# Performance work log

Hardware: AMD Instinct MI355X
Metric: run time of the kernel (lower is better)

The kernel has to match this reference:

```python
import jax, jax.numpy as jnp
import numpy as np

B, T, C = 4, 2048, 1024
H, DQK, DV = 16, 64, 64
W_SCALE = 0.02  # keep logits in a sane range (mimics GPT-style init)


def setup_inputs() -> dict:
    key = jax.random.key(0)
    k1, k2, k3, k4, k5 = jax.random.split(key, 5)
    x = jax.random.normal(k1, (B, T, C), dtype=jnp.float32)
    Wq = jax.random.normal(k2, (C, H * DQK), dtype=jnp.float32) * W_SCALE
    Wk = jax.random.normal(k3, (C, H * DQK), dtype=jnp.float32) * W_SCALE
    Wv = jax.random.normal(k4, (C, H * DV), dtype=jnp.float32) * W_SCALE
    Wp = jax.random.normal(k5, (DV, C), dtype=jnp.float32) * W_SCALE
    return {"x": x, "Wq": Wq, "Wk": Wk, "Wv": Wv, "Wp": Wp, "iter_num": 0}


def reference(x, Wq, Wk, Wv, Wp, iter_num):
    b, t, c = x.shape
    # projections, split into heads: [B, H, T, D]
    q = (x @ Wq).reshape(b, t, H, DQK).transpose(0, 2, 1, 3)
    k = (x @ Wk).reshape(b, t, H, DQK).transpose(0, 2, 1, 3)
    v = (x @ Wv).reshape(b, t, H, DV).transpose(0, 2, 1, 3)
    scale = 1.0 / jnp.sqrt(jnp.asarray(DQK, dtype=x.dtype))
    att = jnp.einsum('bhqd,bhkd->bhqk', q, k) * scale  # [B,H,T,T]
    causal = jnp.tril(jnp.ones((t, t), dtype=bool))
    att = jnp.where(causal[None, None, :, :], att, -jnp.inf)
    att = jax.nn.softmax(att, axis=-1)
    # att @ v then SUM over heads (not concat): [B, T, DV]
    y = jnp.einsum('bhqk,bhkd->bqd', att, v)
    return y @ Wp  # [B, T, C]
```

## Files before the change

kernel.cpp:

```cpp
#include <hip/hip_runtime.h>
#include <hip/hip_bf16.h>

#define DEVI __device__ __forceinline__

typedef __bf16 bf16x8 __attribute__((ext_vector_type(8)));
typedef float f32x4 __attribute__((ext_vector_type(4)));

DEVI unsigned short f2bf(float x) {
    union { __hip_bfloat16 h; unsigned short u; } v;
    v.h = __float2bfloat16(x);
    return v.u;
}

DEVI float exp2_fast(float x) {
#if __has_builtin(__builtin_amdgcn_exp2f)
    return __builtin_amdgcn_exp2f(x);
#else
    return exp2f(x);
#endif
}

DEVI void gload16(const void* gsrc, void* lds) {
    __builtin_amdgcn_global_load_lds(
        (const __attribute__((address_space(1))) void*)gsrc,
        (__attribute__((address_space(3))) void*)lds,
        16, 0, 0);
}

#define BARRIER_MEM() asm volatile("s_barrier" ::: "memory")
#define WAITVM(n) asm volatile("s_waitcnt vmcnt(" #n ")" ::: "memory")
#define LGKM0() asm volatile("s_waitcnt lgkmcnt(0)" ::: "memory")


__global__ __launch_bounds__(256) void convert_f32_bf16_vec(
    const float* __restrict__ in, unsigned short* __restrict__ out, int n4) {
    int i = blockIdx.x * 256 + threadIdx.x;
    if (i >= n4) return;
    float4 v = reinterpret_cast<const float4*>(in)[i];
    ushort4 o;
    o.x = f2bf(v.x); o.y = f2bf(v.y); o.z = f2bf(v.z); o.w = f2bf(v.w);
    reinterpret_cast<ushort4*>(out)[i] = o;
}

__global__ __launch_bounds__(256) void transpose_wqkv(
    const float* __restrict__ wq, const float* __restrict__ wk,
    const float* __restrict__ wv, unsigned short* __restrict__ dst) {
    __shared__ unsigned short tile[32][33];
    const float* src = (blockIdx.z == 0) ? wq : (blockIdx.z == 1) ? wk : wv;
    unsigned short* d = dst + blockIdx.z * 1024 * 1024;
    int c0 = blockIdx.x * 32, r0 = blockIdx.y * 32;
    int tx = threadIdx.x & 31, ty = threadIdx.x >> 5;
    #pragma unroll
    for (int i = ty; i < 32; i += 8)
        tile[tx][i] = f2bf(src[(r0 + i) * 1024 + c0 + tx]);
    __syncthreads();
    #pragma unroll
    for (int i = ty; i < 32; i += 8)
        d[(c0 + i) * 1024 + r0 + tx] = tile[i][tx];
}

__global__ __launch_bounds__(256) void transpose_f32_to_bf16t(
    const float* __restrict__ src, unsigned short* __restrict__ dst,
    int R, int Cc) {
    __shared__ unsigned short tile[32][33];
    int c0 = blockIdx.x * 32, r0 = blockIdx.y * 32;
    int tx = threadIdx.x & 31, ty = threadIdx.x >> 5;
    #pragma unroll
    for (int i = ty; i < 32; i += 8)
        tile[tx][i] = f2bf(src[(r0 + i) * Cc + c0 + tx]);
    __syncthreads();
    #pragma unroll
    for (int i = ty; i < 32; i += 8)
        dst[(c0 + i) * R + r0 + tx] = tile[i][tx];
}

#define LOAD_A8(mh) do { \
    _Pragma("unroll") \
    for (int q = 0; q < 4; ++q) { \
        a[q][0] = *(const bf16x8*)(Arow + ((mh) * 64 + q * 16) * 128 + p16_0); \
        a[q][1] = *(const bf16x8*)(Arow + ((mh) * 64 + q * 16) * 128 + p16_1); \
    } } while (0)

#define LOAD_B4(nh) do { \
    _Pragma("unroll") \
    for (int q2 = 0; q2 < 2; ++q2) { \
        b##nh[q2][0] = *(const bf16x8*)(Brow + ((nh) * 32 + q2 * 16) * 128 + p16_0); \
        b##nh[q2][1] = *(const bf16x8*)(Brow + ((nh) * 32 + q2 * 16) * 128 + p16_1); \
    } } while (0)

#define QUAD(mh, nh) do { \
    __builtin_amdgcn_s_setprio(1); \
    _Pragma("unroll") \
    for (int q = 0; q < 4; ++q) { \
        _Pragma("unroll") \
        for (int q2 = 0; q2 < 2; ++q2) { \
            acc[(mh) * 4 + q][(nh) * 2 + q2] = __builtin_amdgcn_mfma_f32_16x16x32_bf16( \
                a[q][0], b##nh[q2][0], acc[(mh) * 4 + q][(nh) * 2 + q2], 0, 0, 0); \
            acc[(mh) * 4 + q][(nh) * 2 + q2] = __builtin_amdgcn_mfma_f32_16x16x32_bf16( \
                a[q][1], b##nh[q2][1], acc[(mh) * 4 + q][(nh) * 2 + q2], 0, 0, 0); \
        } } \
    __builtin_amdgcn_s_setprio(0); } while (0)

__global__ __launch_bounds__(512, 2) void gemm256(
    const unsigned short* __restrict__ A, const unsigned short* __restrict__ Bt,
    unsigned short* __restrict__ q_out, unsigned short* __restrict__ k_out,
    unsigned short* __restrict__ v_out) {
    __shared__ unsigned short Ab[2][256 * 64];
    __shared__ unsigned short Bb[2][256 * 64];

    const int wg = (blockIdx.x & 7) * 48 + (blockIdx.x >> 3);
    const int bm = (wg / 12) << 8;
    const int bn = (wg % 12) << 8;

    const int tid = threadIdx.x;
    const int w = tid >> 6, l = tid & 63;
    const int wm = w >> 2, wn = w & 3;
    const int lc = l & 15, lg = l >> 4;
    const int lr8 = l >> 3;
    const int colsw = 8 * ((l & 7) ^ lr8);

    const unsigned short* gA = A + (size_t)(bm + lr8) * 1024 + colsw;
    const unsigned short* gB = Bt + (size_t)(bn + lr8) * 1024 + colsw;

    const int p16_0 = ((lg) ^ (lc & 7)) * 16;
    const int p16_1 = ((4 | lg) ^ (lc & 7)) * 16;

    auto STAGE_A = [&](int h, int bufn, int tt) {
        #pragma unroll
        for (int j = 0; j < 2; ++j) {
            const int row0 = wm * 128 + h * 64 + ((((w & 3) << 1) | j) << 3);
            gload16(gA + row0 * 1024 + tt * 64, (char*)&Ab[bufn][0] + row0 * 128);
        }
    };
    auto STAGE_B = [&](int g, int bufn, int tt) {
        #pragma unroll
        for (int j = 0; j < 2; ++j) {
            const int row0 = (w >> 1) * 64 + g * 32 + ((((w & 1) << 1) | j) << 3);
            gload16(gB + row0 * 1024 + tt * 64, (char*)&Bb[bufn][0] + row0 * 128);
        }
    };

    bf16x8 a[4][2], b0[2][2], b1[2][2];
    f32x4 acc[8][4] = {};

    const int nt = 16;

    STAGE_A(0, 0, 0); STAGE_B(0, 0, 0); STAGE_B(1, 0, 0); STAGE_A(1, 0, 0);
    STAGE_A(0, 1, 1); STAGE_B(0, 1, 1); STAGE_B(1, 1, 1);

    #pragma unroll 1
    for (int t = 0; t < nt; ++t) {
        const int buf = t & 1;
        const char* Arow = (const char*)&Ab[buf][0] + (wm * 128 + lc) * 128;
        const char* Brow = (const char*)&Bb[buf][0] + (wn * 64 + lc) * 128;
        if (t == nt - 1) { WAITVM(0); } else { WAITVM(6); }
        BARRIER_MEM();
        LOAD_A8(0);
        LOAD_B4(0);
        if (t + 1 < nt) STAGE_A(1, buf ^ 1, t + 1);
        BARRIER_MEM(); LGKM0();
        QUAD(0, 0);
        BARRIER_MEM();
        LOAD_B4(1);
        if (t + 2 < nt) STAGE_A(0, buf, t + 2);
        BARRIER_MEM(); LGKM0();
        QUAD(0, 1);
        BARRIER_MEM();
        LOAD_A8(1);
        if (t + 2 < nt) STAGE_B(0, buf, t + 2);
        BARRIER_MEM(); LGKM0();
        QUAD(1, 1);
        BARRIER_MEM();
        if (t + 2 < nt) STAGE_B(1, buf, t + 2);
        BARRIER_MEM();
        QUAD(1, 0);
    }

    const int whichsel = bn >> 10;
    const int rrbase = (bn & 1023) + wn * 64 + lc;
    if (whichsel == 2) {
        #pragma unroll
        for (int mi = 0; mi < 8; ++mi) {
            const int m = bm + wm * 128 + mi * 16 + lg * 4;
            const int bb = m >> 11, tt = m & 2047;
            #pragma unroll
            for (int ni = 0; ni < 4; ++ni) {
                const int rr = rrbase + ni * 16;
                const int bhh = bb * 16 + (rr >> 6), d = rr & 63;
                ushort4 o;
                o.x = f2bf(acc[mi][ni][0]); o.y = f2bf(acc[mi][ni][1]);
                o.z = f2bf(acc[mi][ni][2]); o.w = f2bf(acc[mi][ni][3]);
                *reinterpret_cast<ushort4*>(
                    &v_out[((size_t)bhh * 64 + d) * 2048 + tt]) = o;
            }
        }
    } else {
        unsigned short* dst = (whichsel == 0) ? q_out : k_out;
        #pragma unroll
        for (int mi = 0; mi < 8; ++mi) {
            #pragma unroll
            for (int r = 0; r < 4; ++r) {
                const int m = bm + wm * 128 + mi * 16 + lg * 4 + r;
                #pragma unroll
                for (int ni = 0; ni < 4; ++ni)
                    dst[(size_t)m * 1024 + rrbase + ni * 16] = f2bf(acc[mi][ni][r]);
            }
        }
    }
}

template <int EPI>
__global__ __launch_bounds__(256) void gemm_bt(
    const unsigned short* __restrict__ A, const unsigned short* __restrict__ Bt,
    int Mdim, int Ndim, int Kdim,
    unsigned short* __restrict__ q_out, unsigned short* __restrict__ k_out,
    unsigned short* __restrict__ v_out, float* __restrict__ c_out) {
    __shared__ unsigned short As[128 * 32];
    __shared__ unsigned short Bs[128 * 32];
    const int ntn = Ndim >> 7;
    const int bm = (blockIdx.x / ntn) << 7;
    const int bn = (blockIdx.x % ntn) << 7;
    const int tid = threadIdx.x;
    const int w = tid >> 6, l = tid & 63;
    const int wr = w >> 1, wc = w & 1;
    const int lrow = l >> 2, lcb = (l & 3) * 8;
    const int lc = l & 15, lg = l >> 4;

    f32x4 acc[4][4] = {};

    for (int k0 = 0; k0 < Kdim; k0 += 32) {
        __syncthreads();
        #pragma unroll
        for (int i = 0; i < 2; ++i) {
            int j = w * 2 + i;
            gload16(A + (bm + j * 16 + lrow) * Kdim + k0 + lcb, (char*)As + j * 1024);
            gload16(Bt + (bn + j * 16 + lrow) * Kdim + k0 + lcb, (char*)Bs + j * 1024);
        }
        __syncthreads();
        bf16x8 af[4], bfr[4];
        #pragma unroll
        for (int mi = 0; mi < 4; ++mi)
            af[mi] = *reinterpret_cast<const bf16x8*>(&As[(wr * 64 + mi * 16 + lc) * 32 + lg * 8]);
        #pragma unroll
        for (int ni = 0; ni < 4; ++ni)
            bfr[ni] = *reinterpret_cast<const bf16x8*>(&Bs[(wc * 64 + ni * 16 + lc) * 32 + lg * 8]);
        #pragma unroll
        for (int mi = 0; mi < 4; ++mi)
            #pragma unroll
            for (int ni = 0; ni < 4; ++ni)
                acc[mi][ni] = __builtin_amdgcn_mfma_f32_16x16x32_bf16(
                    af[mi], bfr[ni], acc[mi][ni], 0, 0, 0);
    }

    #pragma unroll
    for (int mi = 0; mi < 4; ++mi) {
        #pragma unroll
        for (int ni = 0; ni < 4; ++ni) {
            #pragma unroll
            for (int r = 0; r < 4; ++r) {
                int m = bm + wr * 64 + mi * 16 + lg * 4 + r;
                int n = bn + wc * 64 + ni * 16 + lc;
                float val = acc[mi][ni][r];
                if (EPI == 0) {
                    int which = n >> 10, rr = n & 1023;
                    unsigned short* dst = (which == 0) ? q_out : (which == 1) ? k_out : v_out;
                    dst[m * 1024 + rr] = f2bf(val);
                } else {
                    c_out[m * Ndim + n] = val;
                }
            }
        }
    }
}

__global__ __launch_bounds__(512, 4) void attn_kernel(
    const unsigned short* __restrict__ qb, const unsigned short* __restrict__ kb,
    const unsigned short* __restrict__ vt, unsigned short* __restrict__ ypart) {
    __shared__ unsigned short Ks[3][64 * 64];
    __shared__ unsigned short Vs[3][64 * 64];
    __shared__ unsigned short plds[8][16 * 72];

    const int i = blockIdx.x;
    const int slot = i >> 3;
    const int bh = (i & 7) + ((slot >> 3) << 3);
    const int pr = slot & 7;
    const int b = bh >> 4, h = bh & 15;
    const int tid = threadIdx.x, w = tid >> 6, l = tid & 63;
    const int lc = l & 15, lg = l >> 4;

    const float SCL = 0.125f * 1.44269504f;

    const int rowc = l >> 3;
    const int colsw = 8 * ((l & 7) ^ rowc);
    const unsigned short* kbh = kb + (b * 2048) * 1024 + h * 64;
    const unsigned short* vbh = vt + bh * 64 * 2048;
    const int swz = (lc & 7) * 8;

    unsigned short* pl = &plds[w][0];

    auto STAGE = [&](int bufn, int kt) {
        const int tk0s = kt << 6;
        const int row = w * 8 + rowc;
        gload16(kbh + (tk0s + row) * 1024 + colsw, (char*)&Ks[bufn][0] + w * 1024);
        gload16(vbh + row * 2048 + tk0s + colsw, (char*)&Vs[bufn][0] + w * 1024);
    };

    auto run_pass = [&](int qblk) {
        const int q0 = qblk << 7;
        const int qrowW = q0 + w * 16;

        bf16x8 qf[2];
        {
            const unsigned short* qp =
                qb + (b * 2048 + qrowW + lc) * 1024 + h * 64;
            qf[0] = *reinterpret_cast<const bf16x8*>(qp + lg * 8);
            qf[1] = *reinterpret_cast<const bf16x8*>(qp + 32 + lg * 8);
        }

        f32x4 accO[4] = {};
        float lsum = 0.f;

        const int nkt = 2 * qblk + 2;
        STAGE(0, 0);
        STAGE(1, 1);
        int cur = 0;

        for (int kt = 0; kt < nkt; ++kt) {
            const int tk0 = kt << 6;
            if (kt + 1 < nkt) { WAITVM(2); } else { WAITVM(0); }
            BARRIER_MEM();
            if (kt + 2 < nkt) {
                const int sb = (cur >= 1) ? cur - 1 : cur + 2;
                STAGE(sb, kt + 2);
            }

            if (tk0 <= qrowW + 15) {
                f32x4 s[4] = {};
                #pragma unroll
                for (int ni = 0; ni < 4; ++ni) {
                    const unsigned short* kr = &Ks[cur][(ni * 16 + lc) * 64];
                    bf16x8 kf0 = *reinterpret_cast<const bf16x8*>(&kr[(lg * 8) ^ swz]);
                    bf16x8 kf1 = *reinterpret_cast<const bf16x8*>(&kr[(32 + lg * 8) ^ swz]);
                    s[ni] = __builtin_amdgcn_mfma_f32_16x16x32_bf16(kf0, qf[0], s[ni], 0, 0, 0);
                    s[ni] = __builtin_amdgcn_mfma_f32_16x16x32_bf16(kf1, qf[1], s[ni], 0, 0, 0);
                }
                const bool needmask = (tk0 + 63 > qrowW);
                const int tq = qrowW + lc;
                #pragma unroll
                for (int ni = 0; ni < 4; ++ni) {
                    float pv[4];
                    #pragma unroll
                    for (int r = 0; r < 4; ++r) {
                        float sv = s[ni][r] * SCL;
                        if (needmask) {
                            int tk = tk0 + ni * 16 + lg * 4 + r;
                            sv = (tk > tq) ? -INFINITY : sv;
                        }
                        pv[r] = exp2_fast(sv);
                        lsum += pv[r];
                    }
                    unsigned int w0, w1;
                    asm("v_cvt_pk_bf16_f32 %0, %1, %2" : "=v"(w0) : "v"(pv[0]), "v"(pv[1]));
                    asm("v_cvt_pk_bf16_f32 %0, %1, %2" : "=v"(w1) : "v"(pv[2]), "v"(pv[3]));
                    uint2 pk2; pk2.x = w0; pk2.y = w1;
                    *reinterpret_cast<uint2*>(&pl[lc * 72 + ni * 16 + lg * 4]) = pk2;
                }
                bf16x8 pf0 = *reinterpret_cast<const bf16x8*>(&pl[lc * 72 + lg * 8]);
                bf16x8 pf1 = *reinterpret_cast<const bf16x8*>(&pl[lc * 72 + 32 + lg * 8]);
                #pragma unroll
                for (int ni = 0; ni < 4; ++ni) {
                    const unsigned short* vr = &Vs[cur][(ni * 16 + lc) * 64];
                    bf16x8 vf0 = *reinterpret_cast<const bf16x8*>(&vr[(lg * 8) ^ swz]);
                    bf16x8 vf1 = *reinterpret_cast<const bf16x8*>(&vr[(32 + lg * 8) ^ swz]);
                    accO[ni] = __builtin_amdgcn_mfma_f32_16x16x32_bf16(vf0, pf0, accO[ni], 0, 0, 0);
                    accO[ni] = __builtin_amdgcn_mfma_f32_16x16x32_bf16(vf1, pf1, accO[ni], 0, 0, 0);
                }
            }
            cur = (cur + 1 == 3) ? 0 : cur + 1;
        }
        BARRIER_MEM();

        float tsum = lsum;
        tsum += __shfl_xor(tsum, 16);
        tsum += __shfl_xor(tsum, 32);
        const float rinv = 1.0f / tsum;
        const int tq = qrowW + lc;
        #pragma unroll
        for (int ni = 0; ni < 4; ++ni) {
            ushort4 o;
            o.x = f2bf(accO[ni][0] * rinv);
            o.y = f2bf(accO[ni][1] * rinv);
            o.z = f2bf(accO[ni][2] * rinv);
            o.w = f2bf(accO[ni][3] * rinv);
            *reinterpret_cast<ushort4*>(
                &ypart[(bh * 2048 + tq) * 64 + ni * 16 + lg * 4]) = o;
        }
    };

    run_pass(15 - pr);
    run_pass(pr);
}

__global__ __launch_bounds__(256) void reduce_heads(
    const unsigned short* __restrict__ ypart, unsigned short* __restrict__ yb) {
    int idx = blockIdx.x * 256 + threadIdx.x;
    int d = idx & 63, m = idx >> 6;
    int b = m >> 11, t = m & 2047;
    const unsigned short* p = ypart + ((b * 16) * 2048 + t) * 64 + d;
    float s = 0.f;
    #pragma unroll
    for (int h = 0; h < 16; ++h) {
        union { unsigned short u; __hip_bfloat16 h; } v;
        v.u = p[h * 2048 * 64];
        s += __bfloat162float(v.h);
    }
    yb[idx] = f2bf(s);
}


extern "C" void kernel_launch(void* const* d_in, const int* in_sizes, int n_in,
                              void* d_out, int out_size, void* d_ws, size_t ws_size,
                              hipStream_t stream) {
    const float* x  = (const float*)d_in[0];
    const float* Wq = (const float*)d_in[1];
    const float* Wk = (const float*)d_in[2];
    const float* Wv = (const float*)d_in[3];
    const float* Wp = (const float*)d_in[4];
    float* out = (float*)d_out;

    if (ws_size < 91357184) return;
    char* ws = (char*)d_ws;
    unsigned short* ypart = (unsigned short*)ws;
    unsigned short* xb   = (unsigned short*)ws;
    unsigned short* wt   = (unsigned short*)(ws + 33554432);
    unsigned short* wpt  = (unsigned short*)(ws + 39845888);
    unsigned short* qbf  = (unsigned short*)(ws + 39976960);
    unsigned short* kbf  = (unsigned short*)(ws + 56754176);
    unsigned short* vtb  = (unsigned short*)(ws + 73531392);
    unsigned short* yb   = (unsigned short*)(ws + 90308608);

    convert_f32_bf16_vec<<<8192, 256, 0, stream>>>(x, xb, 2097152);
    transpose_wqkv<<<dim3(32, 32, 3), 256, 0, stream>>>(Wq, Wk, Wv, wt);
    transpose_f32_to_bf16t<<<dim3(32, 2), 256, 0, stream>>>(Wp, wpt, 64, 1024);

    gemm256<<<384, 512, 0, stream>>>(xb, wt, qbf, kbf, vtb);

    attn_kernel<<<512, 512, 0, stream>>>(qbf, kbf, vtb, ypart);

    reduce_heads<<<2048, 256, 0, stream>>>(ypart, yb);

    gemm_bt<1><<<(8192 / 128) * (1024 / 128), 256, 0, stream>>>(
        yb, wpt, 8192, 1024, 64, nullptr, nullptr, nullptr, out);
}
```

Before: 161.4 us.

## Retile QKV GEMM to 256x192 blocks with simple double-buffered loop

Changes the QKV projection GEMM tile from 256x256 to 256x192, so the grid grows from 384 to 512 workgroups (two per CU on a 256-CU part) and the wave layout changes to 4x2 with 64x96 per wave. The fine-grained interleaved staging and compute schedule is replaced by a plain double-buffered loop: wait for all loads, barrier, issue the next tile's loads, then run all MFMAs. The aim is better wave balance across the CUs. In exchange, the tighter overlap between loads and MFMAs is lost, and the full vmcnt(0) wait each iteration may expose memory latency.

After: 155.3 us, median of 2. 3.8% less time.

```diff
diff --git a/kernel.cpp b/kernel.cpp
--- a/kernel.cpp
+++ b/kernel.cpp
@@ -74,47 +74,20 @@
         dst[(c0 + i) * R + r0 + tx] = tile[i][tx];
 }
 
-#define LOAD_A8(mh) do { \
-    _Pragma("unroll") \
-    for (int q = 0; q < 4; ++q) { \
-        a[q][0] = *(const bf16x8*)(Arow + ((mh) * 64 + q * 16) * 128 + p16_0); \
-        a[q][1] = *(const bf16x8*)(Arow + ((mh) * 64 + q * 16) * 128 + p16_1); \
-    } } while (0)
-
-#define LOAD_B4(nh) do { \
-    _Pragma("unroll") \
-    for (int q2 = 0; q2 < 2; ++q2) { \
-        b##nh[q2][0] = *(const bf16x8*)(Brow + ((nh) * 32 + q2 * 16) * 128 + p16_0); \
-        b##nh[q2][1] = *(const bf16x8*)(Brow + ((nh) * 32 + q2 * 16) * 128 + p16_1); \
-    } } while (0)
-
-#define QUAD(mh, nh) do { \
-    __builtin_amdgcn_s_setprio(1); \
-    _Pragma("unroll") \
-    for (int q = 0; q < 4; ++q) { \
-        _Pragma("unroll") \
-        for (int q2 = 0; q2 < 2; ++q2) { \
-            acc[(mh) * 4 + q][(nh) * 2 + q2] = __builtin_amdgcn_mfma_f32_16x16x32_bf16( \
-                a[q][0], b##nh[q2][0], acc[(mh) * 4 + q][(nh) * 2 + q2], 0, 0, 0); \
-            acc[(mh) * 4 + q][(nh) * 2 + q2] = __builtin_amdgcn_mfma_f32_16x16x32_bf16( \
-                a[q][1], b##nh[q2][1], acc[(mh) * 4 + q][(nh) * 2 + q2], 0, 0, 0); \
-        } } \
-    __builtin_amdgcn_s_setprio(0); } while (0)
-
 __global__ __launch_bounds__(512, 2) void gemm256(
     const unsigned short* __restrict__ A, const unsigned short* __restrict__ Bt,
     unsigned short* __restrict__ q_out, unsigned short* __restrict__ k_out,
     unsigned short* __restrict__ v_out) {
     __shared__ unsigned short Ab[2][256 * 64];
-    __shared__ unsigned short Bb[2][256 * 64];
-
-    const int wg = (blockIdx.x & 7) * 48 + (blockIdx.x >> 3);
-    const int bm = (wg / 12) << 8;
-    const int bn = (wg % 12) << 8;
+    __shared__ unsigned short Bb[2][192 * 64];
+
+    const int wg = (blockIdx.x & 7) * 64 + (blockIdx.x >> 3);
+    const int bm = (wg >> 4) << 8;
+    const int bn = (wg & 15) * 192;
 
     const int tid = threadIdx.x;
     const int w = tid >> 6, l = tid & 63;
-    const int wm = w >> 2, wn = w & 3;
+    const int wm = w >> 1, wn = w & 1;
     const int lc = l & 15, lg = l >> 4;
     const int lr8 = l >> 3;
     const int colsw = 8 * ((l & 7) ^ lr8);
@@ -122,89 +95,90 @@
     const unsigned short* gA = A + (size_t)(bm + lr8) * 1024 + colsw;
     const unsigned short* gB = Bt + (size_t)(bn + lr8) * 1024 + colsw;
 
-    const int p16_0 = ((lg) ^ (lc & 7)) * 16;
+    const int p16_0 = (lg ^ (lc & 7)) * 16;
     const int p16_1 = ((4 | lg) ^ (lc & 7)) * 16;
 
-    auto STAGE_A = [&](int h, int bufn, int tt) {
-        #pragma unroll
-        for (int j = 0; j < 2; ++j) {
-            const int row0 = wm * 128 + h * 64 + ((((w & 3) << 1) | j) << 3);
-            gload16(gA + row0 * 1024 + tt * 64, (char*)&Ab[bufn][0] + row0 * 128);
+    auto STAGE = [&](int bufn, int tt) {
+        #pragma unroll
+        for (int j = 0; j < 4; ++j) {
+            const int r0 = j * 64 + w * 8;
+            gload16(gA + (size_t)r0 * 1024 + tt * 64,
+                    (char*)&Ab[bufn][0] + r0 * 128);
+        }
+        #pragma unroll
+        for (int j = 0; j < 3; ++j) {
+            const int r0 = j * 64 + w * 8;
+            gload16(gB + (size_t)r0 * 1024 + tt * 64,
+                    (char*)&Bb[bufn][0] + r0 * 128);
         }
     };
-    auto STAGE_B = [&](int g, int bufn, int tt) {
-        #pragma unroll
-        for (int j = 0; j < 2; ++j) {
-            const int row0 = (w >> 1) * 64 + g * 32 + ((((w & 1) << 1) | j) << 3);
-            gload16(gB + row0 * 1024 + tt * 64, (char*)&Bb[bufn][0] + row0 * 128);
-        }
-    };
-
-    bf16x8 a[4][2], b0[2][2], b1[2][2];
-    f32x4 acc[8][4] = {};
-
+
+    bf16x8 a[4][2], b[6][2];
+    f32x4 acc[4][6] = {};
     const int nt = 16;
 
-    STAGE_A(0, 0, 0); STAGE_B(0, 0, 0); STAGE_B(1, 0, 0); STAGE_A(1, 0, 0);
-    STAGE_A(0, 1, 1); STAGE_B(0, 1, 1); STAGE_B(1, 1, 1);
+    STAGE(0, 0);
 
     #pragma unroll 1
     for (int t = 0; t < nt; ++t) {
         const int buf = t & 1;
-        const char* Arow = (const char*)&Ab[buf][0] + (wm * 128 + lc) * 128;
-        const char* Brow = (const char*)&Bb[buf][0] + (wn * 64 + lc) * 128;
-        if (t == nt - 1) { WAITVM(0); } else { WAITVM(6); }
+        WAITVM(0);
+        LGKM0();
         BARRIER_MEM();
-        LOAD_A8(0);
-        LOAD_B4(0);
-        if (t + 1 < nt) STAGE_A(1, buf ^ 1, t + 1);
-        BARRIER_MEM(); LGKM0();
-        QUAD(0, 0);
-        BARRIER_MEM();
-        LOAD_B4(1);
-        if (t + 2 < nt) STAGE_A(0, buf, t + 2);
-        BARRIER_MEM(); LGKM0();
-        QUAD(0, 1);
-        BARRIER_MEM();
-        LOAD_A8(1);
-        if (t + 2 < nt) STAGE_B(0, buf, t + 2);
-        BARRIER_MEM(); LGKM0();
-        QUAD(1, 1);
-        BARRIER_MEM();
-        if (t + 2 < nt) STAGE_B(1, buf, t + 2);
-        BARRIER_MEM();
-        QUAD(1, 0);
+        if (t + 1 < nt) STAGE(buf ^ 1, t + 1);
+
+        const char* Arow = (const char*)&Ab[buf][0] + (wm * 64 + lc) * 128;
+        const char* Brow = (const char*)&Bb[buf][0] + (wn * 96 + lc) * 128;
+        #pragma unroll
+        for (int fi = 0; fi < 4; ++fi) {
+            a[fi][0] = *(const bf16x8*)(Arow + fi * 16 * 128 + p16_0);
+            a[fi][1] = *(const bf16x8*)(Arow + fi * 16 * 128 + p16_1);
+        }
+        #pragma unroll
+        for (int ni = 0; ni < 6; ++ni) {
+            b[ni][0] = *(const bf16x8*)(Brow + ni * 16 * 128 + p16_0);
+            b[ni][1] = *(const bf16x8*)(Brow + ni * 16 * 128 + p16_1);
+        }
+        __builtin_amdgcn_s_setprio(1);
+        #pragma unroll
+        for (int fi = 0; fi < 4; ++fi)
+            #pragma unroll
+            for (int ni = 0; ni < 6; ++ni) {
+                acc[fi][ni] = __builtin_amdgcn_mfma_f32_16x16x32_bf16(
+                    a[fi][0], b[ni][0], acc[fi][ni], 0, 0, 0);
+                acc[fi][ni] = __builtin_amdgcn_mfma_f32_16x16x32_bf16(
+                    a[fi][1], b[ni][1], acc[fi][ni], 0, 0, 0);
+            }
+        __builtin_amdgcn_s_setprio(0);
     }
 
-    const int whichsel = bn >> 10;
-    const int rrbase = (bn & 1023) + wn * 64 + lc;
-    if (whichsel == 2) {
-        #pragma unroll
-        for (int mi = 0; mi < 8; ++mi) {
-            const int m = bm + wm * 128 + mi * 16 + lg * 4;
-            const int bb = m >> 11, tt = m & 2047;
+    #pragma unroll
+    for (int ni = 0; ni < 6; ++ni) {
+        const int n = bn + wn * 96 + ni * 16 + lc;
+        const int which = n >> 10;
+        const int rr = n & 1023;
+        if (which == 2) {
             #pragma unroll
-            for (int ni = 0; ni < 4; ++ni) {
-                const int rr = rrbase + ni * 16;
-                const int bhh = bb * 16 + (rr >> 6), d = rr & 63;
+            for (int fi = 0; fi < 4; ++fi) {
+                const int m = bm + wm * 64 + fi * 16 + lg * 4;
+                const int bhh = (m >> 11) * 16 + (rr >> 6);
+                const int d = rr & 63;
+                const int tt = m & 2047;
                 ushort4 o;
-                o.x = f2bf(acc[mi][ni][0]); o.y = f2bf(acc[mi][ni][1]);
-                o.z = f2bf(acc[mi][ni][2]); o.w = f2bf(acc[mi][ni][3]);
+                o.x = f2bf(acc[fi][ni][0]); o.y = f2bf(acc[fi][ni][1]);
+                o.z = f2bf(acc[fi][ni][2]); o.w = f2bf(acc[fi][ni][3]);
                 *reinterpret_cast<ushort4*>(
                     &v_out[((size_t)bhh * 64 + d) * 2048 + tt]) = o;
             }
-        }
-    } else {
-        unsigned short* dst = (whichsel == 0) ? q_out : k_out;
-        #pragma unroll
-        for (int mi = 0; mi < 8; ++mi) {
+        } else {
+            unsigned short* dst = which ? k_out : q_out;
             #pragma unroll
-            for (int r = 0; r < 4; ++r) {
-                const int m = bm + wm * 128 + mi * 16 + lg * 4 + r;
+            for (int fi = 0; fi < 4; ++fi)
                 #pragma unroll
-                for (int ni = 0; ni < 4; ++ni)
-                    dst[(size_t)m * 1024 + rrbase + ni * 16] = f2bf(acc[mi][ni][r]);
-            }
+                for (int r = 0; r < 4; ++r) {
+                    const int m = bm + wm * 64 + fi * 16 + lg * 4 + r;
+                    dst[(size_t)m * 1024 + rr] = f2bf(acc[fi][ni][r]);
+                }
         }
     }
 }
@@ -443,7 +417,7 @@
     transpose_wqkv<<<dim3(32, 32, 3), 256, 0, stream>>>(Wq, Wk, Wv, wt);
     transpose_f32_to_bf16t<<<dim3(32, 2), 256, 0, stream>>>(Wp, wpt, 64, 1024);
 
-    gemm256<<<384, 512, 0, stream>>>(xb, wt, qbf, kbf, vtb);
+    gemm256<<<512, 512, 0, stream>>>(xb, wt, qbf, kbf, vtb);
 
     attn_kernel<<<512, 512, 0, stream>>>(qbf, kbf, vtb, ypart);
 
```
